# Kernel optimization log

Measured on AMD Instinct MI355X. Metric: run time of the kernel, lower is better.

The kernel has to match this reference:

```python
import jax, jax.numpy as jnp
import numpy as np

DIM = 768
N_HEADS = 12
HEAD_DIM = DIM // N_HEADS
MLP_MULT = 4
EPS = 1e-5


def setup_inputs() -> dict:
    key = jax.random.key(0)
    ks = jax.random.split(key, 8)
    B, T = 2, 4096
    s = lambda fan_in: 1.0 / np.sqrt(fan_in)
    return {
        "x": jax.random.normal(ks[0], (B, T, DIM), dtype=jnp.float32),
        "ln1_w": jnp.ones((DIM,), jnp.float32),
        "ln1_b": jnp.zeros((DIM,), jnp.float32),
        # weights stored as (in, out): y = x @ W + b (equivalent to torch Linear)
        "w_qkv": jax.random.normal(ks[1], (DIM, 3 * DIM), jnp.float32) * s(DIM),
        "w_proj": jax.random.normal(ks[2], (DIM, DIM), jnp.float32) * s(DIM),
        "b_proj": jnp.zeros((DIM,), jnp.float32),
        "ln2_w": jnp.ones((DIM,), jnp.float32),
        "ln2_b": jnp.zeros((DIM,), jnp.float32),
        "w1": jax.random.normal(ks[3], (DIM, MLP_MULT * DIM), jnp.float32) * s(DIM),
        "b1": jnp.zeros((MLP_MULT * DIM,), jnp.float32),
        "w2": jax.random.normal(ks[4], (MLP_MULT * DIM, DIM), jnp.float32) * s(MLP_MULT * DIM),
        "b2": jnp.zeros((DIM,), jnp.float32),
    }


def _layernorm(x, w, b):
    mean = jnp.mean(x, axis=-1, keepdims=True)
    var = jnp.var(x, axis=-1, keepdims=True)
    return w * (x - mean) * jax.lax.rsqrt(var + EPS) + b


def reference(x, ln1_w, ln1_b, w_qkv, w_proj, b_proj, ln2_w, ln2_b, w1, b1, w2, b2):
    B, T, C = x.shape
    scale = HEAD_DIM ** -0.5

    # --- attention sub-block (pre-LN) ---
    h = _layernorm(x, ln1_w, ln1_b)
    qkv = h @ w_qkv                               # [B, T, 3C]
    q, k, v = jnp.split(qkv, 3, axis=-1)
    to_heads = lambda t: t.reshape(B, T, N_HEADS, HEAD_DIM).transpose(0, 2, 1, 3)
    q, k, v = to_heads(q), to_heads(k), to_heads(v)  # [B, H, T, D]

    att = jnp.einsum("bhqd,bhkd->bhqk", q, k) * scale  # full T x T scores
    causal = jnp.tril(jnp.ones((T, T), dtype=bool))
    att = jnp.where(causal, att, -jnp.inf)
    att = jax.nn.softmax(att, axis=-1)
    y = jnp.einsum("bhqk,bhkd->bhqd", att, v)          # [B, H, T, D]
    y = y.transpose(0, 2, 1, 3).reshape(B, T, C)
    y = y @ w_proj + b_proj
    x = x + y

    # --- MLP sub-block (pre-LN) ---
    h = _layernorm(x, ln2_w, ln2_b)
    h = jax.nn.gelu(h @ w1 + b1, approximate=False)
    h = h @ w2 + b2
    return x + h
```

## Files before the change

kernel.cpp:

```cpp
#include <hip/hip_runtime.h>

typedef unsigned short u16;
typedef __attribute__((ext_vector_type(4))) unsigned short u16x4;
typedef __attribute__((ext_vector_type(8))) short short8;
typedef __attribute__((ext_vector_type(4))) float f32x4;
typedef __attribute__((ext_vector_type(16))) float f32x16;

#define MFMA32(a, b, c) __builtin_amdgcn_mfma_f32_32x32x16_bf16(a, b, c, 0, 0, 0)

__device__ __forceinline__ u16 f2bf(float f) {
  union { float f; unsigned u; } x; x.f = f;
  unsigned r = x.u + 0x7fffu + ((x.u >> 16) & 1u);
  return (u16)(r >> 16);
}

__device__ __forceinline__ unsigned cvt_pk_bf16(float lo, float hi) {
  unsigned r;
  asm("v_cvt_pk_bf16_f32 %0, %1, %2" : "=v"(r) : "v"(lo), "v"(hi));
  return r;
}

__device__ __forceinline__ void load_lds16(const void* g, void* l) {
  __builtin_amdgcn_global_load_lds(
      (const __attribute__((address_space(1))) void*)g,
      (__attribute__((address_space(3))) void*)l,
      16, 0, 0);
}

__global__ __launch_bounds__(256) void transpose_k(const float* __restrict__ in,
                                                   u16* __restrict__ out,
                                                   int R, int C) {
  __shared__ float tile[32][33];
  const int tx = threadIdx.x & 31, ty = threadIdx.x >> 5;
  const int c0 = blockIdx.x * 32, r0 = blockIdx.y * 32;
#pragma unroll
  for (int i = 0; i < 4; ++i)
    tile[ty + i * 8][tx] = in[(size_t)(r0 + ty + i * 8) * C + c0 + tx];
  __syncthreads();
#pragma unroll
  for (int i = 0; i < 4; ++i)
    out[(size_t)(c0 + ty + i * 8) * R + r0 + tx] = f2bf(tile[tx][ty + i * 8]);
}

__global__ __launch_bounds__(256) void ln_k(const float* __restrict__ X,
                                            const float* __restrict__ w,
                                            const float* __restrict__ b,
                                            u16* __restrict__ O) {
  const int row = blockIdx.x;
  const float* xr = X + (size_t)row * 768;
  const int tid = threadIdx.x;
  float v0 = xr[tid], v1 = xr[tid + 256], v2 = xr[tid + 512];
  float s = v0 + v1 + v2;
  float s2 = v0 * v0 + v1 * v1 + v2 * v2;
#pragma unroll
  for (int m = 32; m; m >>= 1) { s += __shfl_xor(s, m); s2 += __shfl_xor(s2, m); }
  __shared__ float ps[4], ps2[4];
  if ((tid & 63) == 0) { ps[tid >> 6] = s; ps2[tid >> 6] = s2; }
  __syncthreads();
  s = ps[0] + ps[1] + ps[2] + ps[3];
  s2 = ps2[0] + ps2[1] + ps2[2] + ps2[3];
  const float mean = s * (1.f / 768.f);
  const float var = s2 * (1.f / 768.f) - mean * mean;
  const float rstd = rsqrtf(var + 1e-5f);
  u16* orow = O + (size_t)row * 768;
  orow[tid]       = f2bf((v0 - mean) * rstd * w[tid]       + b[tid]);
  orow[tid + 256] = f2bf((v1 - mean) * rstd * w[tid + 256] + b[tid + 256]);
  orow[tid + 512] = f2bf((v2 - mean) * rstd * w[tid + 512] + b[tid + 512]);
}

#define BM 128
#define BN 128
#define BKK 64

template <int EPI>
__global__ __launch_bounds__(256, 2) void gemm_k(
    const u16* __restrict__ A, const u16* __restrict__ Bt, int K, int N,
    const float* __restrict__ bias, const float* __restrict__ res,
    float* __restrict__ outF, u16* __restrict__ outB,
    u16* __restrict__ qout, u16* __restrict__ kout, u16* __restrict__ vout) {
  __shared__ __align__(16) u16 sA[BM * BKK];
  __shared__ __align__(16) u16 sB[BN * BKK];
  const int nTn = N / BN;
  const int nwg = gridDim.x;
  const int bid = ((int)blockIdx.x & 7) * (nwg >> 3) + ((int)blockIdx.x >> 3);
  const int tm = bid / nTn, tn = bid % nTn;
  const int m0 = tm * BM, n0 = tn * BN;
  const int tid = threadIdx.x, lane = tid & 63, wv = tid >> 6;
  const int wr = wv >> 1, wc = wv & 1;
  const int fr = lane & 15, fg = lane >> 4;

  const u16* aSrc[4];
  const u16* bSrc[4];
#pragma unroll
  for (int i = 0; i < 4; ++i) {
    int f = (i * 4 + wv) * 64 + lane;
    int r = f >> 3;
    int c = (f & 7) ^ (r & 7);
    aSrc[i] = A + (size_t)(m0 + r) * K + c * 8;
    bSrc[i] = Bt + (size_t)(n0 + r) * K + c * 8;
  }

  f32x4 acc[4][4];
#pragma unroll
  for (int m = 0; m < 4; ++m)
#pragma unroll
    for (int n = 0; n < 4; ++n) acc[m][n] = f32x4{0.f, 0.f, 0.f, 0.f};

  const int aswz = fr & 7;
  for (int kt = 0; kt < K; kt += BKK) {
#pragma unroll
    for (int i = 0; i < 4; ++i) {
      load_lds16(aSrc[i] + kt, (char*)sA + (i * 4 + wv) * 1024);
      load_lds16(bSrc[i] + kt, (char*)sB + (i * 4 + wv) * 1024);
    }
    __syncthreads();
#pragma unroll
    for (int ks = 0; ks < 2; ++ks) {
      const int c16 = (ks * 4 + fg) ^ aswz;
      short8 af[4], bf[4];
#pragma unroll
      for (int m = 0; m < 4; ++m)
        af[m] = *(const short8*)((const char*)sA +
                                 (((wr * 64 + m * 16 + fr) * 8 + c16) << 4));
#pragma unroll
      for (int n = 0; n < 4; ++n)
        bf[n] = *(const short8*)((const char*)sB +
                                 (((wc * 64 + n * 16 + fr) * 8 + c16) << 4));
#pragma unroll
      for (int m = 0; m < 4; ++m)
#pragma unroll
        for (int n = 0; n < 4; ++n)
          acc[m][n] =
              __builtin_amdgcn_mfma_f32_16x16x32_bf16(af[m], bf[n], acc[m][n], 0, 0, 0);
    }
    __syncthreads();
  }

#pragma unroll
  for (int m = 0; m < 4; ++m) {
    const int row = m0 + wr * 64 + m * 16 + fg * 4;
#pragma unroll
    for (int n = 0; n < 4; ++n) {
      const int col = n0 + wc * 64 + n * 16 + fr;
      f32x4 v = acc[m][n];
      if (EPI == 0) {
        const int part = (col >= 1536) ? 2 : (col >= 768 ? 1 : 0);
        const int cc = col - part * 768;
        const int hh = cc >> 6, dd = cc & 63;
        const int bb = row >> 12;
        const int t = row & 4095;
        const size_t bhh = (size_t)(bb * 12 + hh);
        if (part == 2) {
          const int ks_ = (t & 63) >> 4, h_ = (t >> 3) & 1, e0 = t & 7;
          u16x4 pk = {f2bf(v[0]), f2bf(v[1]), f2bf(v[2]), f2bf(v[3])};
          *(u16x4*)(vout + bhh * 262144 + (size_t)(t >> 6) * 4096 +
                    (size_t)(((ks_ << 2) + ((dd >> 5) << 1) + h_) * 256 +
                             (dd & 31) * 8 + e0)) = pk;
        } else if (part == 1) {
          const int ks_ = dd >> 4, h_ = (dd >> 3) & 1, e = dd & 7;
          u16* base = kout + bhh * 262144;
#pragma unroll
          for (int r = 0; r < 4; ++r) {
            const int t2 = t + r;
            base[(size_t)(t2 >> 6) * 4096 +
                 (size_t)((((ks_ << 2) + (((t2 & 63) >> 5) << 1) + h_) * 256) +
                          (t2 & 31) * 8 + e)] = f2bf(v[r]);
          }
        } else {
          const float qs = 0.18033688011112042f;
          u16* dst = qout + (bhh * 4096 + t) * 64 + dd;
#pragma unroll
          for (int r = 0; r < 4; ++r) dst[(size_t)r * 64] = f2bf(v[r] * qs);
        }
      } else if (EPI == 1) {
        const float bv = bias[col];
#pragma unroll
        for (int r = 0; r < 4; ++r)
          outF[(size_t)(row + r) * N + col] =
              v[r] + bv + res[(size_t)(row + r) * N + col];
      } else {
        const float bv = bias[col];
#pragma unroll
        for (int r = 0; r < 4; ++r) {
          float t = v[r] + bv;
          float g = 0.5f * t * (1.f + erff(t * 0.70710678118654752f));
          outB[(size_t)(row + r) * N + col] = f2bf(g);
        }
      }
    }
  }
}

__global__ __launch_bounds__(256, 2) void gemm64_k(
    const u16* __restrict__ A, const u16* __restrict__ Bt, int K, int N,
    const float* __restrict__ bias, const float* __restrict__ res,
    float* __restrict__ outF) {
  __shared__ __align__(16) u16 sA[128 * 64];
  __shared__ __align__(16) u16 sB[64 * 64];
  const int nTn = N / 64;
  const int nwg = gridDim.x;
  const int bid = ((int)blockIdx.x & 7) * (nwg >> 3) + ((int)blockIdx.x >> 3);
  const int tm = bid / nTn, tn = bid % nTn;
  const int m0 = tm * 128, n0 = tn * 64;
  const int tid = threadIdx.x, lane = tid & 63, wv = tid >> 6;
  const int fr = lane & 15, fg = lane >> 4;

  const u16* aSrc[4];
  const u16* bSrc[2];
#pragma unroll
  for (int i = 0; i < 4; ++i) {
    const int f = i * 256 + tid;
    const int r = f >> 3;
    const int c = (f & 7) ^ (r & 7);
    aSrc[i] = A + (size_t)(m0 + r) * K + c * 8;
  }
#pragma unroll
  for (int i = 0; i < 2; ++i) {
    const int f = i * 256 + tid;
    const int r = f >> 3;
    const int c = (f & 7) ^ (r & 7);
    bSrc[i] = Bt + (size_t)(n0 + r) * K + c * 8;
  }

  f32x4 acc[2][4];
#pragma unroll
  for (int m = 0; m < 2; ++m)
#pragma unroll
    for (int n = 0; n < 4; ++n) acc[m][n] = f32x4{0.f, 0.f, 0.f, 0.f};

  const int aswz = fr & 7;
  for (int kt = 0; kt < K; kt += 64) {
#pragma unroll
    for (int i = 0; i < 4; ++i)
      load_lds16(aSrc[i] + kt, (char*)sA + (i * 256 + tid) * 16);
#pragma unroll
    for (int i = 0; i < 2; ++i)
      load_lds16(bSrc[i] + kt, (char*)sB + (i * 256 + tid) * 16);
    __syncthreads();
#pragma unroll
    for (int ks = 0; ks < 2; ++ks) {
      const int c16 = (ks * 4 + fg) ^ aswz;
      short8 af[2], bf[4];
#pragma unroll
      for (int m = 0; m < 2; ++m)
        af[m] = *(const short8*)((const char*)sA +
                                 (((wv * 32 + m * 16 + fr) * 8 + c16) << 4));
#pragma unroll
      for (int n = 0; n < 4; ++n)
        bf[n] = *(const short8*)((const char*)sB +
                                 (((n * 16 + fr) * 8 + c16) << 4));
#pragma unroll
      for (int m = 0; m < 2; ++m)
#pragma unroll
        for (int n = 0; n < 4; ++n)
          acc[m][n] =
              __builtin_amdgcn_mfma_f32_16x16x32_bf16(af[m], bf[n], acc[m][n], 0, 0, 0);
    }
    __syncthreads();
  }

#pragma unroll
  for (int m = 0; m < 2; ++m) {
    const int row = m0 + wv * 32 + m * 16 + fg * 4;
#pragma unroll
    for (int n = 0; n < 4; ++n) {
      const int col = n0 + n * 16 + fr;
      const float bv = bias[col];
      f32x4 v = acc[m][n];
#pragma unroll
      for (int r = 0; r < 4; ++r)
        outF[(size_t)(row + r) * N + col] =
            v[r] + bv + res[(size_t)(row + r) * N + col];
    }
  }
}

__global__ __launch_bounds__(256) void attn_k(const u16* __restrict__ Q,
                                              const u16* __restrict__ Kb,
                                              const u16* __restrict__ Vt,
                                              u16* __restrict__ Y) {
  __shared__ __align__(16) u16 sK[2][8192];
  __shared__ __align__(16) u16 sV[2][8192];
  const int bid = blockIdx.x;
  const int qt = 31 - bid / 24;
  const int bh = bid % 24;
  const int bb = bh / 12, hh = bh - bb * 12;
  const int tid = threadIdx.x, lane = tid & 63, wv = tid >> 6;
  const int l31 = lane & 31, hi = lane >> 5;
  const int wq0 = qt * 128 + wv * 32;
  const int qG = wq0 + l31;
  const u16* Qh = Q + (size_t)bh * 4096 * 64;
  const u16* Kh = Kb + (size_t)bh * 262144;
  const u16* Vh = Vt + (size_t)bh * 262144;

  short8 qf[4];
#pragma unroll
  for (int ks = 0; ks < 4; ++ks)
    qf[ks] = *(const short8*)(Qh + (size_t)qG * 64 + ks * 16 + hi * 8);

  f32x16 yacc[2];
  yacc[0] = (f32x16)0.f;
  yacc[1] = (f32x16)0.f;
  float lrun = 0.f;

#define STAGE(buf, cc)                                                         \
  do {                                                                         \
    const u16* gk_ = Kh + (size_t)(cc)*8192;                                   \
    const u16* gv_ = Vh + (size_t)(cc)*8192;                                   \
    _Pragma("unroll") for (int i_ = 0; i_ < 4; ++i_) {                         \
      const int f_ = i_ * 256 + tid;                                           \
      load_lds16(gk_ + f_ * 8, (char*)sK[buf] + f_ * 16);                      \
      load_lds16(gv_ + f_ * 8, (char*)sV[buf] + f_ * 16);                      \
    }                                                                          \
  } while (0)

  const int nch = qt + 1;
  STAGE(0, 0);
  __syncthreads();

  const int rdBase = hi * 512 + l31 * 16;

  for (int c = 0; c < nch; ++c) {
    const int cur = c & 1;
    if (c + 1 < nch) STAGE(cur ^ 1, c + 1);

#pragma unroll
    for (int hf = 0; hf < 2; ++hf) {
      const int kb = c * 128 + hf * 64;
      if (kb <= wq0 + 31) {
        const char* sKb = (const char*)sK[cur] + hf * 8192;
        const char* sVb = (const char*)sV[cur] + hf * 8192;

        f32x16 s[2];
        s[0] = (f32x16)0.f;
        s[1] = (f32x16)0.f;
        __builtin_amdgcn_s_setprio(1);
#pragma unroll
        for (int ks = 0; ks < 4; ++ks) {
#pragma unroll
          for (int kc = 0; kc < 2; ++kc) {
            short8 kf = *(const short8*)(sKb + ks * 2048 + kc * 1024 + rdBase);
            s[kc] = MFMA32(kf, qf[ks], s[kc]);
          }
        }
        __builtin_amdgcn_s_setprio(0);

        if (kb + 63 > wq0) {
#pragma unroll
          for (int kc = 0; kc < 2; ++kc)
#pragma unroll
            for (int r = 0; r < 16; ++r) {
              const int key = kb + kc * 32 + (r & 3) + 8 * (r >> 2) + 4 * hi;
              if (key > qG) s[kc][r] = -3e38f;
            }
        }

#pragma unroll
        for (int kc = 0; kc < 2; ++kc)
#pragma unroll
          for (int r = 0; r < 16; ++r)
            s[kc][r] = __builtin_amdgcn_exp2f(s[kc][r] - 8.f);

        float u[8];
#pragma unroll
        for (int i = 0; i < 8; ++i)
          u[i] = (s[0][i] + s[0][i + 8]) + (s[1][i] + s[1][i + 8]);
#pragma unroll
        for (int st = 4; st; st >>= 1)
#pragma unroll
          for (int i = 0; i < st; ++i) u[i] += u[i + st];
        lrun += u[0] + __shfl_xor(u[0], 32);

#pragma unroll
        for (int ks2 = 0; ks2 < 4; ++ks2) {
          const int kc = ks2 >> 1, rb = (ks2 & 1) * 8;
          unsigned W0 = cvt_pk_bf16(s[kc][rb + 0], s[kc][rb + 1]);
          unsigned W1 = cvt_pk_bf16(s[kc][rb + 2], s[kc][rb + 3]);
          unsigned W2 = cvt_pk_bf16(s[kc][rb + 4], s[kc][rb + 5]);
          unsigned W3 = cvt_pk_bf16(s[kc][rb + 6], s[kc][rb + 7]);
          asm("v_permlane32_swap_b32 %0, %1" : "+v"(W0), "+v"(W2));
          asm("v_permlane32_swap_b32 %0, %1" : "+v"(W1), "+v"(W3));
          union { unsigned w[4]; short8 v; } pb;
          pb.w[0] = W0; pb.w[1] = W1; pb.w[2] = W2; pb.w[3] = W3;
          __builtin_amdgcn_s_setprio(1);
#pragma unroll
          for (int dt = 0; dt < 2; ++dt) {
            short8 vf = *(const short8*)(sVb + ks2 * 2048 + dt * 1024 + rdBase);
            yacc[dt] = MFMA32(vf, pb.v, yacc[dt]);
          }
          __builtin_amdgcn_s_setprio(0);
        }
      }
    }
    __syncthreads();
  }

  const float inv = 1.f / lrun;
  u16* Yr = Y + (size_t)(bb * 4096 + qt * 128 + wv * 32 + l31) * 768 + hh * 64;
#pragma unroll
  for (int dt = 0; dt < 2; ++dt)
#pragma unroll
    for (int g = 0; g < 4; ++g) {
      u16x4 pk = {f2bf(yacc[dt][g * 4 + 0] * inv), f2bf(yacc[dt][g * 4 + 1] * inv),
                  f2bf(yacc[dt][g * 4 + 2] * inv), f2bf(yacc[dt][g * 4 + 3] * inv)};
      *(u16x4*)(Yr + dt * 32 + g * 8 + hi * 4) = pk;
    }
#undef STAGE
}

extern "C" void kernel_launch(void* const* d_in, const int* in_sizes, int n_in,
                              void* d_out, int out_size, void* d_ws, size_t ws_size,
                              hipStream_t stream) {
  const float* x = (const float*)d_in[0];
  const float* ln1w = (const float*)d_in[1];
  const float* ln1b = (const float*)d_in[2];
  const float* wqkv = (const float*)d_in[3];
  const float* wproj = (const float*)d_in[4];
  const float* bproj = (const float*)d_in[5];
  const float* ln2w = (const float*)d_in[6];
  const float* ln2b = (const float*)d_in[7];
  const float* w1 = (const float*)d_in[8];
  const float* b1 = (const float*)d_in[9];
  const float* w2 = (const float*)d_in[10];
  const float* b2 = (const float*)d_in[11];
  float* out = (float*)d_out;
  char* ws = (char*)d_ws;

  const size_t SZ_ACT = (size_t)8192 * 768 * 2;
  u16* hbuf = (u16*)(ws);
  u16* qb = (u16*)(ws + SZ_ACT);
  u16* kb = (u16*)(ws + 2 * SZ_ACT);
  u16* vT = (u16*)(ws + 3 * SZ_ACT);
  u16* ybuf = (u16*)(ws + 4 * SZ_ACT);
  float* out1 = (float*)(ws + 5 * SZ_ACT);
  char* wsw = ws + 5 * SZ_ACT + (size_t)8192 * 768 * 4;
  u16* wqkvT = (u16*)(wsw);
  u16* wprojT = (u16*)(wsw + 3538944);
  u16* w1T = (u16*)(wsw + 3538944 + 1179648);
  u16* w2T = (u16*)(wsw + 3538944 + 1179648 + 4718592);
  u16* h3 = hbuf;
  u16* h2 = ybuf;

  transpose_k<<<dim3(2304 / 32, 768 / 32), 256, 0, stream>>>(wqkv, wqkvT, 768, 2304);
  transpose_k<<<dim3(768 / 32, 768 / 32), 256, 0, stream>>>(wproj, wprojT, 768, 768);
  transpose_k<<<dim3(3072 / 32, 768 / 32), 256, 0, stream>>>(w1, w1T, 768, 3072);
  transpose_k<<<dim3(768 / 32, 3072 / 32), 256, 0, stream>>>(w2, w2T, 3072, 768);

  ln_k<<<8192, 256, 0, stream>>>(x, ln1w, ln1b, hbuf);

  gemm_k<0><<<64 * (2304 / 128), 256, 0, stream>>>(hbuf, wqkvT, 768, 2304,
      nullptr, nullptr, nullptr, nullptr, qb, kb, vT);

  attn_k<<<768, 256, 0, stream>>>(qb, kb, vT, ybuf);

  gemm64_k<<<64 * (768 / 64), 256, 0, stream>>>(ybuf, wprojT, 768, 768,
      bproj, x, out1);

  ln_k<<<8192, 256, 0, stream>>>(out1, ln2w, ln2b, h2);

  gemm_k<2><<<64 * (3072 / 128), 256, 0, stream>>>(h2, w1T, 768, 3072,
      b1, nullptr, nullptr, h3, nullptr, nullptr, nullptr);

  gemm64_k<<<64 * (768 / 64), 256, 0, stream>>>(h3, w2T, 3072, 768,
      b2, out1, out);

  (void)in_sizes; (void)n_in; (void)out_size; (void)ws_size;
}
```

Before: 272.1 us.

## Double-buffer LDS tiles in GEMM kernels to overlap loads with MFMA

Both GEMM kernels now use two LDS buffers for the A and B tiles. The next K-tile is prefetched via global_load_lds while the current tile feeds the MFMAs, hiding global memory latency behind compute. This doubles LDS usage per block, which may reduce occupancy, and relies on the barrier's wait semantics for correctness of the async loads.

```diff
diff --git a/kernel.cpp b/kernel.cpp
--- a/kernel.cpp
+++ b/kernel.cpp
@@ -78,8 +78,8 @@
     const float* __restrict__ bias, const float* __restrict__ res,
     float* __restrict__ outF, u16* __restrict__ outB,
     u16* __restrict__ qout, u16* __restrict__ kout, u16* __restrict__ vout) {
-  __shared__ __align__(16) u16 sA[BM * BKK];
-  __shared__ __align__(16) u16 sB[BN * BKK];
+  __shared__ __align__(16) u16 sA[2][BM * BKK];
+  __shared__ __align__(16) u16 sB[2][BN * BKK];
   const int nTn = N / BN;
   const int nwg = gridDim.x;
   const int bid = ((int)blockIdx.x & 7) * (nwg >> 3) + ((int)blockIdx.x >> 3);
@@ -100,6 +100,14 @@
     bSrc[i] = Bt + (size_t)(n0 + r) * K + c * 8;
   }
 
+#define GSTAGE(buf, kt)                                                        \
+  do {                                                                         \
+    _Pragma("unroll") for (int i_ = 0; i_ < 4; ++i_) {                         \
+      load_lds16(aSrc[i_] + (kt), (char*)sA[buf] + (i_ * 4 + wv) * 1024);      \
+      load_lds16(bSrc[i_] + (kt), (char*)sB[buf] + (i_ * 4 + wv) * 1024);      \
+    }                                                                          \
+  } while (0)
+
   f32x4 acc[4][4];
 #pragma unroll
   for (int m = 0; m < 4; ++m)
@@ -107,24 +115,24 @@
     for (int n = 0; n < 4; ++n) acc[m][n] = f32x4{0.f, 0.f, 0.f, 0.f};
 
   const int aswz = fr & 7;
-  for (int kt = 0; kt < K; kt += BKK) {
-#pragma unroll
-    for (int i = 0; i < 4; ++i) {
-      load_lds16(aSrc[i] + kt, (char*)sA + (i * 4 + wv) * 1024);
-      load_lds16(bSrc[i] + kt, (char*)sB + (i * 4 + wv) * 1024);
-    }
-    __syncthreads();
+  const int nkt = K / BKK;
+  GSTAGE(0, 0);
+  __syncthreads();
+
+  for (int t = 0; t < nkt; ++t) {
+    const int cur = t & 1;
+    if (t + 1 < nkt) GSTAGE(cur ^ 1, (t + 1) * BKK);
 #pragma unroll
     for (int ks = 0; ks < 2; ++ks) {
       const int c16 = (ks * 4 + fg) ^ aswz;
       short8 af[4], bf[4];
 #pragma unroll
       for (int m = 0; m < 4; ++m)
-        af[m] = *(const short8*)((const char*)sA +
+        af[m] = *(const short8*)((const char*)sA[cur] +
                                  (((wr * 64 + m * 16 + fr) * 8 + c16) << 4));
 #pragma unroll
       for (int n = 0; n < 4; ++n)
-        bf[n] = *(const short8*)((const char*)sB +
+        bf[n] = *(const short8*)((const char*)sB[cur] +
                                  (((wc * 64 + n * 16 + fr) * 8 + c16) << 4));
 #pragma unroll
       for (int m = 0; m < 4; ++m)
@@ -135,6 +143,7 @@
     }
     __syncthreads();
   }
+#undef GSTAGE
 
 #pragma unroll
   for (int m = 0; m < 4; ++m) {
@@ -195,8 +204,8 @@
     const u16* __restrict__ A, const u16* __restrict__ Bt, int K, int N,
     const float* __restrict__ bias, const float* __restrict__ res,
     float* __restrict__ outF) {
-  __shared__ __align__(16) u16 sA[128 * 64];
-  __shared__ __align__(16) u16 sB[64 * 64];
+  __shared__ __align__(16) u16 sA[2][128 * 64];
+  __shared__ __align__(16) u16 sB[2][64 * 64];
   const int nTn = N / 64;
   const int nwg = gridDim.x;
   const int bid = ((int)blockIdx.x & 7) * (nwg >> 3) + ((int)blockIdx.x >> 3);
@@ -222,6 +231,14 @@
     bSrc[i] = Bt + (size_t)(n0 + r) * K + c * 8;
   }
 
+#define GSTAGE64(buf, kt)                                                      \
+  do {                                                                         \
+    _Pragma("unroll") for (int i_ = 0; i_ < 4; ++i_)                           \
+        load_lds16(aSrc[i_] + (kt), (char*)sA[buf] + (i_ * 256 + tid) * 16);   \
+    _Pragma("unroll") for (int i_ = 0; i_ < 2; ++i_)                           \
+        load_lds16(bSrc[i_] + (kt), (char*)sB[buf] + (i_ * 256 + tid) * 16);   \
+  } while (0)
+
   f32x4 acc[2][4];
 #pragma unroll
   for (int m = 0; m < 2; ++m)
@@ -229,25 +246,24 @@
     for (int n = 0; n < 4; ++n) acc[m][n] = f32x4{0.f, 0.f, 0.f, 0.f};
 
   const int aswz = fr & 7;
-  for (int kt = 0; kt < K; kt += 64) {
-#pragma unroll
-    for (int i = 0; i < 4; ++i)
-      load_lds16(aSrc[i] + kt, (char*)sA + (i * 256 + tid) * 16);
-#pragma unroll
-    for (int i = 0; i < 2; ++i)
-      load_lds16(bSrc[i] + kt, (char*)sB + (i * 256 + tid) * 16);
-    __syncthreads();
+  const int nkt = K / 64;
+  GSTAGE64(0, 0);
+  __syncthreads();
+
+  for (int t = 0; t < nkt; ++t) {
+    const int cur = t & 1;
+    if (t + 1 < nkt) GSTAGE64(cur ^ 1, (t + 1) * 64);
 #pragma unroll
     for (int ks = 0; ks < 2; ++ks) {
       const int c16 = (ks * 4 + fg) ^ aswz;
       short8 af[2], bf[4];
 #pragma unroll
       for (int m = 0; m < 2; ++m)
-        af[m] = *(const short8*)((const char*)sA +
+        af[m] = *(const short8*)((const char*)sA[cur] +
                                  (((wv * 32 + m * 16 + fr) * 8 + c16) << 4));
 #pragma unroll
       for (int n = 0; n < 4; ++n)
-        bf[n] = *(const short8*)((const char*)sB +
+        bf[n] = *(const short8*)((const char*)sB[cur] +
                                  (((n * 16 + fr) * 8 + c16) << 4));
 #pragma unroll
       for (int m = 0; m < 2; ++m)
@@ -258,6 +274,7 @@
     }
     __syncthreads();
   }
+#undef GSTAGE64
 
 #pragma unroll
   for (int m = 0; m < 2; ++m) {
```

Result: slower. 295.7 us (+8.7%).
